# Kernel optimization log

Hardware: AMD Instinct MI355X
Metric: run time of the kernel (lower is better)

Reference implementation:

```python
import jax, jax.numpy as jnp
import numpy as np
import math

EPS = 1e-5  # torch LayerNorm default


def entmax15(z):
    # Peters & Martins exact sort-based alpha=1.5 entmax along last axis.
    z = z / 2.0
    z = z - jnp.max(z, axis=-1, keepdims=True)
    zs = -jnp.sort(-z, axis=-1)                      # descending
    K = z.shape[-1]
    rho = jnp.arange(1, K + 1, dtype=z.dtype)
    mean = jnp.cumsum(zs, axis=-1) / rho
    mean_sq = jnp.cumsum(zs * zs, axis=-1) / rho
    ss = rho * (mean_sq - mean * mean)
    delta = jnp.clip((1.0 - ss) / rho, 0.0)
    tau = mean - jnp.sqrt(delta)
    k = jnp.sum(tau <= zs, axis=-1, keepdims=True)   # support size
    tau_star = jnp.take_along_axis(tau, k - 1, axis=-1)
    p = jnp.square(jnp.clip(z - tau_star, 0.0))
    return p


def mish(x):
    return x * jnp.tanh(jax.nn.softplus(x))


def layer_norm(x, g, b):
    mu = jnp.mean(x, axis=-1, keepdims=True)
    var = jnp.var(x, axis=-1, keepdims=True)
    return (x - mu) / jnp.sqrt(var + EPS) * g + b


def setup_inputs() -> dict:
    key = jax.random.key(0)
    D, H, F = 512, 8, 2048
    B, S = 8, 1024
    ks = jax.random.split(key, 16)
    s = 1.0 / math.sqrt(D)
    inp = {
        "x": jax.random.normal(ks[0], (B, S, D), jnp.float32),
        # weights stored [in, out]; y = x @ W + b
        "Wq": jax.random.normal(ks[1], (D, D), jnp.float32) * s,
        "bq": jnp.zeros((D,), jnp.float32),
        "Wk": jax.random.normal(ks[2], (D, D), jnp.float32) * s,
        "bk": jnp.zeros((D,), jnp.float32),
        "Wv": jax.random.normal(ks[3], (D, D), jnp.float32) * s,
        "bv": jnp.zeros((D,), jnp.float32),
        "Wo": jax.random.normal(ks[4], (D, D), jnp.float32) * s,
        "bo": jnp.zeros((D,), jnp.float32),
        "g1": jnp.ones((D,), jnp.float32),
        "be1": jnp.zeros((D,), jnp.float32),
        "W1": jax.random.normal(ks[5], (D, F), jnp.float32) * s,
        "b1": jnp.zeros((F,), jnp.float32),
        "W2": jax.random.normal(ks[6], (F, D), jnp.float32) * (1.0 / math.sqrt(F)),
        "b2": jnp.zeros((D,), jnp.float32),
        "g2": jnp.ones((D,), jnp.float32),
        "be2": jnp.zeros((D,), jnp.float32),
    }
    return inp


def reference(x, Wq, bq, Wk, bk, Wv, bv, Wo, bo, g1, be1, W1, b1, W2, b2, g2, be2):
    B, S, D = x.shape
    H = 8
    hd = D // H
    # multi-head self-attention (z = x)
    q = (x @ Wq + bq).reshape(B, S, H, hd).transpose(0, 2, 1, 3)
    k = (x @ Wk + bk).reshape(B, S, H, hd).transpose(0, 2, 1, 3)
    v = (x @ Wv + bv).reshape(B, S, H, hd).transpose(0, 2, 1, 3)
    scores = jnp.einsum("bhqd,bhkd->bhqk", q, k) / math.sqrt(hd)
    attn = entmax15(scores)
    out = jnp.einsum("bhqk,bhkd->bhqd", attn, v)
    out = out.transpose(0, 2, 1, 3).reshape(B, S, D)
    y = out @ Wo + bo
    x = x + layer_norm(y, g1, be1)
    # feed-forward with Mish
    y = mish(x @ W1 + b1) @ W2 + b2
    x = x + layer_norm(y, g2, be2)
    return x
```

## Files before the change

### kernel.cpp

```cpp
#include <hip/hip_runtime.h>


typedef float f32x4 __attribute__((ext_vector_type(4)));
typedef float f32x2 __attribute__((ext_vector_type(2)));
typedef __bf16 b8 __attribute__((ext_vector_type(8)));

#define DEV static __device__ __forceinline__

DEV unsigned short f2bf(float f) {
  return __builtin_bit_cast(unsigned short, (__bf16)f);
}
DEV float bf2f(unsigned short b) { return __uint_as_float(((unsigned)b) << 16); }

DEV float mishf(float x) {
  if (x > 20.f) return x;
  float e = __expf(x);
  float u = 1.f + e;
  u *= u;
  return x * ((u - 1.f) / (u + 1.f));
}

DEV void async16(const void* g, void* l) {
  __builtin_amdgcn_global_load_lds(
      (const __attribute__((address_space(1))) unsigned int*)g,
      (__attribute__((address_space(3))) unsigned int*)l, 16, 0, 0);
}

DEV int mbcnt64(unsigned long long m) {
  return __builtin_amdgcn_mbcnt_hi((unsigned)(m >> 32),
                                   __builtin_amdgcn_mbcnt_lo((unsigned)m, 0));
}

template <int CTRL>
DEV float dppmov(float x) {
  return __builtin_bit_cast(
      float, __builtin_amdgcn_update_dpp(0, __builtin_bit_cast(int, x), CTRL,
                                         0xF, 0xF, true));
}
DEV float swz16(float x) {
  return __builtin_bit_cast(
      float, __builtin_amdgcn_ds_swizzle(__builtin_bit_cast(int, x), 0x401F));
}
DEV float wave_sum(float x) {
  x += dppmov<0xB1>(x);
  x += dppmov<0x4E>(x);
  x += dppmov<0x141>(x);
  x += dppmov<0x140>(x);
  x += swz16(x);
  x += __shfl_xor(x, 32);
  return x;
}
DEV float wave_max(float x) {
  x = fmaxf(x, dppmov<0xB1>(x));
  x = fmaxf(x, dppmov<0x4E>(x));
  x = fmaxf(x, dppmov<0x141>(x));
  x = fmaxf(x, dppmov<0x140>(x));
  x = fmaxf(x, swz16(x));
  x = fmaxf(x, __shfl_xor(x, 32));
  return x;
}

template <int WM, int WN, int EPI, bool OUTBF, bool DB>
__global__ __launch_bounds__(256) void gemm_bt(
    const unsigned short* __restrict__ A, const unsigned short* __restrict__ Bt,
    const float* __restrict__ bias, void* __restrict__ Cp,
    int K, int lda, int ldb, int ldc,
    long sA1, long sA2, long sB1, long sB2, long sC1, long sC2,
    int hdiv, float alpha) {
  constexpr int BM = WM * 64, BN = WN * 64;
  constexpr int NA = WM * 2, NB = WN * 2;
  constexpr int NBUF = DB ? 2 : 1;
  __shared__ unsigned short smA[NBUF * BM * 64];
  __shared__ unsigned short smB[NBUF * BN * 64];

  const int tid = threadIdx.x;
  const int lane = tid & 63;
  const int z = blockIdx.z;
  const long zi = z / hdiv, zr = z % hdiv;
  const unsigned short* Ab = A + zi * sA1 + zr * sA2 + (long)blockIdx.x * BM * lda;
  const unsigned short* Bb = Bt + zi * sB1 + zr * sB2 + (long)blockIdx.y * BN * ldb;

  int siA[NA];
  const unsigned short* gA[NA];
#pragma unroll
  for (int q = 0; q < NA; ++q) {
    int si = q * 256 + tid;
    int m = si >> 3, s = si & 7, g = s ^ (m & 7);
    siA[q] = si;
    gA[q] = Ab + (long)m * lda + g * 8;
  }
  int siB[NB];
  const unsigned short* gB[NB];
#pragma unroll
  for (int q = 0; q < NB; ++q) {
    int si = q * 256 + tid;
    int m = si >> 3, s = si & 7, g = s ^ (m & 7);
    siB[q] = si;
    gB[q] = Bb + (long)m * ldb + g * 8;
  }

  const int w = tid >> 6;
  const int wr = w / WN, wc = w % WN;
  const int fm = lane & 15, fg = lane >> 4;

  int aOff[4][2], bOff[4][2];
#pragma unroll
  for (int i = 0; i < 4; ++i)
#pragma unroll
    for (int ks = 0; ks < 2; ++ks) {
      int m = wr * 64 + i * 16 + fm;
      aOff[i][ks] = (m * 8 + ((ks * 4 + fg) ^ (fm & 7))) * 8;
      int n = wc * 64 + i * 16 + fm;
      bOff[i][ks] = (n * 8 + ((ks * 4 + fg) ^ (fm & 7))) * 8;
    }

  f32x4 acc[4][4];
#pragma unroll
  for (int i = 0; i < 4; ++i)
#pragma unroll
    for (int j = 0; j < 4; ++j) acc[i][j] = (f32x4){0.f, 0.f, 0.f, 0.f};

  auto stage = [&](int buf, int k0) {
    unsigned short* dA = smA + buf * (BM * 64);
    unsigned short* dB = smB + buf * (BN * 64);
#pragma unroll
    for (int q = 0; q < NA; ++q) async16(gA[q] + k0, (void*)&dA[siA[q] * 8]);
#pragma unroll
    for (int q = 0; q < NB; ++q) async16(gB[q] + k0, (void*)&dB[siB[q] * 8]);
  };
  auto compute = [&](int buf) {
    const unsigned short* sA = smA + buf * (BM * 64);
    const unsigned short* sB = smB + buf * (BN * 64);
#pragma unroll
    for (int ks = 0; ks < 2; ++ks) {
      b8 aF[4], bF[4];
#pragma unroll
      for (int i = 0; i < 4; ++i) aF[i] = *(const b8*)&sA[aOff[i][ks]];
#pragma unroll
      for (int j = 0; j < 4; ++j) bF[j] = *(const b8*)&sB[bOff[j][ks]];
#pragma unroll
      for (int i = 0; i < 4; ++i)
#pragma unroll
        for (int j = 0; j < 4; ++j)
          acc[i][j] = __builtin_amdgcn_mfma_f32_16x16x32_bf16(aF[i], bF[j], acc[i][j], 0, 0, 0);
    }
  };

  if constexpr (DB) {
    stage(0, 0);
    __syncthreads();
    int cur = 0;
    for (int k0 = 64; k0 < K; k0 += 64) {
      stage(cur ^ 1, k0);
      compute(cur);
      __syncthreads();
      cur ^= 1;
    }
    compute(cur);
  } else {
    for (int k0 = 0; k0 < K; k0 += 64) {
      __syncthreads();
      stage(0, k0);
      __syncthreads();
      compute(0);
    }
  }

  const long cbase = zi * sC1 + zr * sC2;
  const int row0 = blockIdx.x * BM + wr * 64 + fg * 4;
  const int col0 = blockIdx.y * BN + wc * 64 + fm;
#pragma unroll
  for (int i = 0; i < 4; ++i) {
#pragma unroll
    for (int j = 0; j < 4; ++j) {
      const int col = col0 + j * 16;
      float bv = (EPI >= 1) ? bias[col] : 0.f;
#pragma unroll
      for (int r = 0; r < 4; ++r) {
        const int row = row0 + i * 16 + r;
        float v = acc[i][j][r] * alpha + bv;
        if (EPI == 2) v = mishf(v);
        const long idx = cbase + (long)row * ldc + col;
        if constexpr (OUTBF)
          ((unsigned short*)Cp)[idx] = f2bf(v);
        else
          ((float*)Cp)[idx] = v;
      }
    }
  }
}

template <int NC>
DEV float solve_tau(const f32x2* zc, float tau) {
  int kprev = -1;
  const f32x2 zero2 = (f32x2){0.f, 0.f};
  for (int it = 0; it < 12; ++it) {
    const f32x2 t2 = (f32x2){tau, tau};
    f32x2 s1v = zero2, s2v = zero2;
    int k = 0;
#pragma unroll
    for (int i = 0; i < NC; ++i) {
      f32x2 h = zc[i] - t2;
      k += __popcll(__ballot(h.x > 0.f));
      k += __popcll(__ballot(h.y > 0.f));
      f32x2 hp = __builtin_elementwise_max(h, zero2);
      s1v += hp;
      s2v += hp * hp;
    }
    float s1 = wave_sum(s1v.x + s1v.y);
    float s2 = wave_sum(s2v.x + s2v.y);
    if (k == kprev) break;
    kprev = k;
    float kf = (float)k;
    float disc = fmaxf(fmaf(s1, s1, -kf * (s2 - 1.f)), 0.f);
    tau += (s1 - __builtin_sqrtf(disc)) / kf;
  }
  return tau;
}

DEV float solve_tau_lds(const float* cw, int nch, int lane, float tau) {
  int kprev = -1;
  const f32x2 zero2 = (f32x2){0.f, 0.f};
  for (int it = 0; it < 12; ++it) {
    const f32x2 t2 = (f32x2){tau, tau};
    f32x2 s1v = zero2, s2v = zero2;
    int k = 0;
    for (int c = 0; c < nch; ++c) {
      f32x2 h = *(const f32x2*)&cw[c * 128 + lane * 2] - t2;
      k += __popcll(__ballot(h.x > 0.f));
      k += __popcll(__ballot(h.y > 0.f));
      f32x2 hp = __builtin_elementwise_max(h, zero2);
      s1v += hp;
      s2v += hp * hp;
    }
    float s1 = wave_sum(s1v.x + s1v.y);
    float s2 = wave_sum(s2v.x + s2v.y);
    if (k == kprev) break;
    kprev = k;
    float kf = (float)k;
    float disc = fmaxf(fmaf(s1, s1, -kf * (s2 - 1.f)), 0.f);
    tau += (s1 - __builtin_sqrtf(disc)) / kf;
  }
  return tau;
}

__global__ __launch_bounds__(256) void entmax_rows(unsigned short* __restrict__ P) {
  const int tid = threadIdx.x, lane = tid & 63, wv = tid >> 6;
  const long row = (long)blockIdx.x * 4 + wv;
  unsigned short* p = P + row * 1024;
  __shared__ float cand[4][1024];

  union { uint4 v; unsigned short u[8]; } a, b;
  a.v = *(const uint4*)(p + lane * 16);
  b.v = *(const uint4*)(p + lane * 16 + 8);
  f32x2 zp[8];
#pragma unroll
  for (int i = 0; i < 4; ++i) {
    zp[i] = (f32x2){bf2f(a.u[2 * i]), bf2f(a.u[2 * i + 1])};
    zp[4 + i] = (f32x2){bf2f(b.u[2 * i]), bf2f(b.u[2 * i + 1])};
  }

  f32x2 mv = zp[0];
#pragma unroll
  for (int i = 1; i < 8; ++i) mv = __builtin_elementwise_max(mv, zp[i]);
  float m = wave_max(fmaxf(mv.x, mv.y));

  const float thr = m - 1.f;
  float* cw = cand[wv];

  int base = 0;
#pragma unroll
  for (int i = 0; i < 8; ++i) {
    unsigned long long mx = __ballot(zp[i].x > thr);
    if (zp[i].x > thr) cw[base + mbcnt64(mx)] = zp[i].x;
    base += __popcll(mx);
    unsigned long long my = __ballot(zp[i].y > thr);
    if (zp[i].y > thr) cw[base + mbcnt64(my)] = zp[i].y;
    base += __popcll(my);
  }

  const int nch = (base + 127) >> 7;
  for (int i = base + lane; i < nch * 128; i += 64) cw[i] = -1e30f;

  float tau;
  if (nch == 1) {
    f32x2 zc[1];
    zc[0] = *(const f32x2*)&cw[lane * 2];
    tau = solve_tau<1>(zc, thr);
  } else if (nch == 2) {
    f32x2 zc[2];
    zc[0] = *(const f32x2*)&cw[lane * 2];
    zc[1] = *(const f32x2*)&cw[128 + lane * 2];
    tau = solve_tau<2>(zc, thr);
  } else {
    tau = solve_tau_lds(cw, nch, lane, thr);
  }

  const f32x2 t2 = (f32x2){tau, tau};
  const f32x2 zero2 = (f32x2){0.f, 0.f};
#pragma unroll
  for (int i = 0; i < 4; ++i) {
    f32x2 h0 = __builtin_elementwise_max(zp[i] - t2, zero2);
    f32x2 h1 = __builtin_elementwise_max(zp[4 + i] - t2, zero2);
    f32x2 p0 = h0 * h0, p1 = h1 * h1;
    a.u[2 * i] = f2bf(p0.x);
    a.u[2 * i + 1] = f2bf(p0.y);
    b.u[2 * i] = f2bf(p1.x);
    b.u[2 * i + 1] = f2bf(p1.y);
  }
  *(uint4*)(p + lane * 16) = a.v;
  *(uint4*)(p + lane * 16 + 8) = b.v;
}

__global__ __launch_bounds__(256) void prep_all(
    const float* __restrict__ x, unsigned short* __restrict__ xb,
    const float* __restrict__ Wq, const float* __restrict__ Wk,
    const float* __restrict__ Wv, const float* __restrict__ Wo,
    const float* __restrict__ W1, const float* __restrict__ W2,
    unsigned short* __restrict__ Wqkvt, unsigned short* __restrict__ Wot,
    unsigned short* __restrict__ W1t, unsigned short* __restrict__ W2t,
    const float* __restrict__ bq, const float* __restrict__ bk,
    const float* __restrict__ bv, float* __restrict__ bqkv) {
  __shared__ float t[32][33];
  const int bid = blockIdx.x, tid = threadIdx.x;

  if (bid < 4096) {
    long i = ((long)bid * 256 + tid) * 4;
    float4 v = *(const float4*)&x[i];
    uint2 pk;
    pk.x = (unsigned)f2bf(v.x) | ((unsigned)f2bf(v.y) << 16);
    pk.y = (unsigned)f2bf(v.z) | ((unsigned)f2bf(v.w) << 16);
    *(uint2*)&xb[i] = pk;
    return;
  }

  const float* in;
  unsigned short* out;
  int ldi, ldo, bx, by;
  if (bid < 5120) {
    int t4 = (bid - 4096) >> 8, local = (bid - 4096) & 255;
    const float* ins[4] = {Wq, Wk, Wv, Wo};
    unsigned short* outs[4] = {Wqkvt, Wqkvt + 512 * 512, Wqkvt + 2 * 512 * 512, Wot};
    in = ins[t4];
    out = outs[t4];
    ldi = 512;
    ldo = 512;
    bx = local & 15;
    by = local >> 4;
  } else if (bid < 6144) {
    int local = bid - 5120;
    in = W1;
    out = W1t;
    ldi = 2048;
    ldo = 512;
    bx = local & 63;
    by = local >> 6;
  } else if (bid < 7168) {
    int local = bid - 6144;
    in = W2;
    out = W2t;
    ldi = 512;
    ldo = 2048;
    bx = local & 15;
    by = local >> 4;
  } else {
    int i = (bid - 7168) * 256 + tid;
    if (i < 512) bqkv[i] = bq[i];
    else if (i < 1024) bqkv[i] = bk[i - 512];
    else if (i < 1536) bqkv[i] = bv[i - 1024];
    return;
  }

  const int tx = tid & 31, ty = tid >> 5;
  const int r0 = by * 32, c0 = bx * 32;
#pragma unroll
  for (int q = 0; q < 4; ++q) {
    int r = ty + q * 8;
    t[r][tx] = in[(long)(r0 + r) * ldi + c0 + tx];
  }
  __syncthreads();
#pragma unroll
  for (int q = 0; q < 4; ++q) {
    int r = ty + q * 8;
    out[(long)(c0 + r) * ldo + r0 + tx] = f2bf(t[tx][r]);
  }
}

__global__ __launch_bounds__(256) void transpose_b2b(const unsigned short* __restrict__ in,
                                                     unsigned short* __restrict__ out,
                                                     int ldi, int ldo, long i1, long i2,
                                                     long o1, long o2, int hdiv) {
  __shared__ unsigned short t[32][33];
  const int z = blockIdx.z;
  in += (long)(z / hdiv) * i1 + (long)(z % hdiv) * i2;
  out += (long)(z / hdiv) * o1 + (long)(z % hdiv) * o2;
  const int tx = threadIdx.x & 31, ty = threadIdx.x >> 5;
  const int r0 = blockIdx.y * 32, c0 = blockIdx.x * 32;
#pragma unroll
  for (int q = 0; q < 4; ++q) {
    int r = ty + q * 8;
    t[r][tx] = in[(long)(r0 + r) * ldi + c0 + tx];
  }
  __syncthreads();
#pragma unroll
  for (int q = 0; q < 4; ++q) {
    int r = ty + q * 8;
    out[(long)(c0 + r) * ldo + r0 + tx] = t[tx][r];
  }
}

template <bool WB, int NS>
__global__ __launch_bounds__(256) void ln_res(const float* __restrict__ xin,
                                              const float* __restrict__ y, long ystr,
                                              const float* __restrict__ ybias,
                                              const float* __restrict__ g,
                                              const float* __restrict__ be,
                                              float* __restrict__ xo,
                                              unsigned short* __restrict__ xob) {
  const int row = blockIdx.x, tid = threadIdx.x, lane = tid & 63, wv = tid >> 6;
  const long base = (long)row * 512 + tid * 2;
  const int c = tid * 2;
  float2 v = *(const float2*)&y[base];
#pragma unroll
  for (int j = 1; j < NS; ++j) {
    float2 u = *(const float2*)&y[base + j * ystr];
    v.x += u.x;
    v.y += u.y;
  }
  v.x += ybias[c];
  v.y += ybias[c + 1];
  float s1 = wave_sum(v.x + v.y);
  float s2 = wave_sum(v.x * v.x + v.y * v.y);
  __shared__ float red[4][2];
  if (lane == 0) {
    red[wv][0] = s1;
    red[wv][1] = s2;
  }
  __syncthreads();
  s1 = red[0][0] + red[1][0] + red[2][0] + red[3][0];
  s2 = red[0][1] + red[1][1] + red[2][1] + red[3][1];
  const float mu = s1 * (1.f / 512.f);
  const float rstd = rsqrtf(s2 * (1.f / 512.f) - mu * mu + 1e-5f);
  float2 xv = *(const float2*)&xin[base];
  float o0 = xv.x + (v.x - mu) * rstd * g[c] + be[c];
  float o1 = xv.y + (v.y - mu) * rstd * g[c + 1] + be[c + 1];
  float2 ov;
  ov.x = o0;
  ov.y = o1;
  *(float2*)&xo[base] = ov;
  if constexpr (WB) {
    unsigned pk = (unsigned)f2bf(o0) | ((unsigned)f2bf(o1) << 16);
    *(unsigned*)&xob[base] = pk;
  }
}

extern "C" void kernel_launch(void* const* d_in, const int* in_sizes, int n_in,
                              void* d_out, int out_size, void* d_ws, size_t ws_size,
                              hipStream_t stream) {
  const int B = 8, S = 1024, D = 512, H = 8, F = 2048;
  const int BS = B * S;
  const int N3 = 3 * D;

  const float* x = (const float*)d_in[0];
  const float* Wq = (const float*)d_in[1];
  const float* bq = (const float*)d_in[2];
  const float* Wk = (const float*)d_in[3];
  const float* bk = (const float*)d_in[4];
  const float* Wv = (const float*)d_in[5];
  const float* bv = (const float*)d_in[6];
  const float* Wo = (const float*)d_in[7];
  const float* bo = (const float*)d_in[8];
  const float* g1 = (const float*)d_in[9];
  const float* be1 = (const float*)d_in[10];
  const float* W1 = (const float*)d_in[11];
  const float* b1 = (const float*)d_in[12];
  const float* W2 = (const float*)d_in[13];
  const float* b2 = (const float*)d_in[14];
  const float* g2 = (const float*)d_in[15];
  const float* be2 = (const float*)d_in[16];
  float* out = (float*)d_out;

  char* w = (char*)d_ws;
  size_t off = 0;
  auto alloc = [&](size_t bytes) -> void* {
    void* p = w + off;
    off += bytes;
    off = (off + 255) & ~(size_t)255;
    return p;
  };

  unsigned short* xb = (unsigned short*)alloc((size_t)BS * D * 2);
  unsigned short* Wqkvt = (unsigned short*)alloc((size_t)N3 * D * 2);
  unsigned short* Wot = (unsigned short*)alloc((size_t)D * D * 2);
  unsigned short* W1t = (unsigned short*)alloc((size_t)F * D * 2);
  unsigned short* W2t = (unsigned short*)alloc((size_t)D * F * 2);
  float* bqkv = (float*)alloc((size_t)N3 * 4);
  unsigned short* QKVb = (unsigned short*)alloc((size_t)BS * N3 * 2);
  unsigned short* Vt = (unsigned short*)alloc((size_t)BS * D * 2);
  unsigned short* attn = (unsigned short*)alloc((size_t)BS * D * 2);
  unsigned short* P = (unsigned short*)alloc((size_t)B * H * S * S * 2);
  float* x1 = (float*)alloc((size_t)BS * D * 4);
  unsigned short* hb = (unsigned short*)alloc((size_t)BS * F * 2);
  unsigned short* x1b = xb;
  float* yp = (float*)P;
  const long PSTR = (long)BS * D;

  const long SS = (long)S * S;
  const long HSS = (long)H * SS;

  prep_all<<<7174, 256, 0, stream>>>(x, xb, Wq, Wk, Wv, Wo, W1, W2,
                                     Wqkvt, Wot, W1t, W2t, bq, bk, bv, bqkv);

  gemm_bt<2, 2, 1, true, true><<<dim3(BS / 128, N3 / 128, 1), 256, 0, stream>>>(
      xb, Wqkvt, bqkv, QKVb, D, D, D, N3, 0, 0, 0, 0, 0, 0, 1, 1.f);

  transpose_b2b<<<dim3(2, 32, 64), 256, 0, stream>>>(
      QKVb + 1024, Vt, N3, S, (long)S * N3, 64, (long)8 * 64 * S, (long)64 * S, 8);

  gemm_bt<2, 2, 0, true, false><<<dim3(S / 128, S / 128, B * H), 256, 0, stream>>>(
      QKVb, QKVb + 512, nullptr, P, 64, N3, N3, S,
      (long)S * N3, 64, (long)S * N3, 64, HSS, SS, H, 1.f / 16.f);

  entmax_rows<<<(B * H * S) / 4, 256, 0, stream>>>(P);

  gemm_bt<4, 1, 0, true, true><<<dim3(S / 256, 1, B * H), 256, 0, stream>>>(
      P, Vt, nullptr, attn, S, S, S, D,
      HSS, SS, (long)8 * 64 * S, (long)64 * S, (long)S * D, 64, H, 1.f);

  gemm_bt<2, 2, 0, false, true><<<dim3(BS / 128, D / 128, 2), 256, 0, stream>>>(
      attn, Wot, nullptr, yp, D / 2, D, D, D, 0, D / 2, 0, D / 2, 0, PSTR, 2, 1.f);

  ln_res<true, 2><<<BS, 256, 0, stream>>>(x, yp, PSTR, bo, g1, be1, x1, x1b);

  gemm_bt<2, 2, 2, true, true><<<dim3(BS / 128, F / 128, 1), 256, 0, stream>>>(
      x1b, W1t, b1, hb, D, D, D, F, 0, 0, 0, 0, 0, 0, 1, 1.f);

  gemm_bt<2, 2, 0, false, true><<<dim3(BS / 128, D / 128, 2), 256, 0, stream>>>(
      hb, W2t, nullptr, yp, F / 2, F, F, D, 0, F / 2, 0, F / 2, 0, PSTR, 2, 1.f);

  ln_res<false, 2><<<BS, 256, 0, stream>>>(x1, yp, PSTR, b2, g2, be2, out, nullptr);
}
```

Baseline: 355.5 us.

## Fuse entmax probability transform into PV GEMM A-operand load

The entmax kernel now only solves for tau per row and writes it to a small buffer, instead of rewriting the full bf16 score matrix with the probabilities. A new PV GEMM reads the raw scores through registers, applies (z - tau)^2 clamped at zero while staging them into LDS, and multiplies with V. This removes one full write pass over the 128 MB score matrix. In exchange the A operand goes through registers rather than async LDS loads, which adds register pressure and ALU work inside the GEMM loop. The template flag on several other gemm_bt launches also changes, presumably a loading-mode choice.

```diff
diff --git a/kernel.cpp b/kernel.cpp
--- a/kernel.cpp
+++ b/kernel.cpp
@@ -185,6 +185,135 @@
           ((unsigned short*)Cp)[idx] = f2bf(v);
         else
           ((float*)Cp)[idx] = v;
+      }
+    }
+  }
+}
+
+__global__ __launch_bounds__(256) void gemm_pv(
+    const unsigned short* __restrict__ P, const unsigned short* __restrict__ Vt,
+    const float* __restrict__ Tau, unsigned short* __restrict__ attn) {
+  constexpr int BM = 256, BN = 64;
+  constexpr int NA = 8, NB = 2;
+  __shared__ unsigned short smA[2 * BM * 64];
+  __shared__ unsigned short smB[2 * BN * 64];
+
+  const int tid = threadIdx.x;
+  const int lane = tid & 63;
+  const int z = blockIdx.z;
+  const long SS = 1024L * 1024L;
+  const unsigned short* Ab = P + (long)z * SS + (long)blockIdx.x * BM * 1024;
+  const unsigned short* Bb = Vt + (long)z * 64 * 1024;
+  const float* Tb = Tau + (long)z * 1024 + blockIdx.x * BM;
+
+  int siA[NA];
+  const unsigned short* gA[NA];
+  float tq[NA];
+#pragma unroll
+  for (int q = 0; q < NA; ++q) {
+    int si = q * 256 + tid;
+    int m = si >> 3, s = si & 7, g = s ^ (m & 7);
+    siA[q] = si;
+    gA[q] = Ab + (long)m * 1024 + g * 8;
+    tq[q] = Tb[m];
+  }
+  int siB[NB];
+  const unsigned short* gB[NB];
+#pragma unroll
+  for (int q = 0; q < NB; ++q) {
+    int si = q * 256 + tid;
+    int m = si >> 3, s = si & 7, g = s ^ (m & 7);
+    siB[q] = si;
+    gB[q] = Bb + (long)m * 1024 + g * 8;
+  }
+
+  const int w = tid >> 6;
+  const int fm = lane & 15, fg = lane >> 4;
+  int aOff[4][2], bOff[4][2];
+#pragma unroll
+  for (int i = 0; i < 4; ++i)
+#pragma unroll
+    for (int ks = 0; ks < 2; ++ks) {
+      int m = w * 64 + i * 16 + fm;
+      aOff[i][ks] = (m * 8 + ((ks * 4 + fg) ^ (fm & 7))) * 8;
+      int n = i * 16 + fm;
+      bOff[i][ks] = (n * 8 + ((ks * 4 + fg) ^ (fm & 7))) * 8;
+    }
+
+  f32x4 acc[4][4];
+#pragma unroll
+  for (int i = 0; i < 4; ++i)
+#pragma unroll
+    for (int j = 0; j < 4; ++j) acc[i][j] = (f32x4){0.f, 0.f, 0.f, 0.f};
+
+  union AB { b8 v; unsigned short u[8]; };
+  AB areg[NA];
+  auto loadA = [&](int k0) {
+#pragma unroll
+    for (int q = 0; q < NA; ++q) areg[q].v = *(const b8*)(gA[q] + k0);
+  };
+  auto xformA = [&](int buf) {
+    unsigned short* dA = smA + buf * (BM * 64);
+#pragma unroll
+    for (int q = 0; q < NA; ++q) {
+      AB o;
+#pragma unroll
+      for (int e = 0; e < 8; ++e) {
+        float h = fmaxf(bf2f(areg[q].u[e]) - tq[q], 0.f);
+        o.u[e] = f2bf(h * h);
+      }
+      *(b8*)&dA[siA[q] * 8] = o.v;
+    }
+  };
+  auto stageB = [&](int buf, int k0) {
+    unsigned short* dB = smB + buf * (BN * 64);
+#pragma unroll
+    for (int q = 0; q < NB; ++q) async16(gB[q] + k0, (void*)&dB[siB[q] * 8]);
+  };
+  auto compute = [&](int buf) {
+    const unsigned short* sA = smA + buf * (BM * 64);
+    const unsigned short* sB = smB + buf * (BN * 64);
+#pragma unroll
+    for (int ks = 0; ks < 2; ++ks) {
+      b8 aF[4], bF[4];
+#pragma unroll
+      for (int i = 0; i < 4; ++i) aF[i] = *(const b8*)&sA[aOff[i][ks]];
+#pragma unroll
+      for (int j = 0; j < 4; ++j) bF[j] = *(const b8*)&sB[bOff[j][ks]];
+#pragma unroll
+      for (int i = 0; i < 4; ++i)
+#pragma unroll
+        for (int j = 0; j < 4; ++j)
+          acc[i][j] = __builtin_amdgcn_mfma_f32_16x16x32_bf16(aF[i], bF[j], acc[i][j], 0, 0, 0);
+    }
+  };
+
+  loadA(0);
+  stageB(0, 0);
+  xformA(0);
+  __syncthreads();
+  int cur = 0;
+  for (int k0 = 64; k0 < 1024; k0 += 64) {
+    loadA(k0);
+    stageB(cur ^ 1, k0);
+    compute(cur);
+    xformA(cur ^ 1);
+    __syncthreads();
+    cur ^= 1;
+  }
+  compute(cur);
+
+  const long cbase = (long)(z >> 3) * 1024 * 512 + (z & 7) * 64;
+  const int row0 = blockIdx.x * BM + w * 64 + fg * 4;
+#pragma unroll
+  for (int i = 0; i < 4; ++i) {
+#pragma unroll
+    for (int j = 0; j < 4; ++j) {
+      const int col = fm + j * 16;
+#pragma unroll
+      for (int r = 0; r < 4; ++r) {
+        const int row = row0 + i * 16 + r;
+        attn[cbase + (long)row * 512 + col] = f2bf(acc[i][j][r]);
       }
     }
   }
@@ -244,10 +373,11 @@
   return tau;
 }
 
-__global__ __launch_bounds__(256) void entmax_rows(unsigned short* __restrict__ P) {
+__global__ __launch_bounds__(256) void entmax_tau(const unsigned short* __restrict__ P,
+                                                  float* __restrict__ T) {
   const int tid = threadIdx.x, lane = tid & 63, wv = tid >> 6;
   const long row = (long)blockIdx.x * 4 + wv;
-  unsigned short* p = P + row * 1024;
+  const unsigned short* p = P + row * 1024;
   __shared__ float cand[4][1024];
 
   union { uint4 v; unsigned short u[8]; } a, b;
@@ -296,20 +426,7 @@
     tau = solve_tau_lds(cw, nch, lane, thr);
   }
 
-  const f32x2 t2 = (f32x2){tau, tau};
-  const f32x2 zero2 = (f32x2){0.f, 0.f};
-#pragma unroll
-  for (int i = 0; i < 4; ++i) {
-    f32x2 h0 = __builtin_elementwise_max(zp[i] - t2, zero2);
-    f32x2 h1 = __builtin_elementwise_max(zp[4 + i] - t2, zero2);
-    f32x2 p0 = h0 * h0, p1 = h1 * h1;
-    a.u[2 * i] = f2bf(p0.x);
-    a.u[2 * i + 1] = f2bf(p0.y);
-    b.u[2 * i] = f2bf(p1.x);
-    b.u[2 * i + 1] = f2bf(p1.y);
-  }
-  *(uint4*)(p + lane * 16) = a.v;
-  *(uint4*)(p + lane * 16 + 8) = b.v;
+  if (lane == 0) T[row] = tau;
 }
 
 __global__ __launch_bounds__(256) void prep_all(
@@ -499,6 +616,7 @@
   unsigned short* Vt = (unsigned short*)alloc((size_t)BS * D * 2);
   unsigned short* attn = (unsigned short*)alloc((size_t)BS * D * 2);
   unsigned short* P = (unsigned short*)alloc((size_t)B * H * S * S * 2);
+  float* Tau = (float*)alloc((size_t)B * H * S * 4);
   float* x1 = (float*)alloc((size_t)BS * D * 4);
   unsigned short* hb = (unsigned short*)alloc((size_t)BS * F * 2);
   unsigned short* x1b = xb;
@@ -511,7 +629,7 @@
   prep_all<<<7174, 256, 0, stream>>>(x, xb, Wq, Wk, Wv, Wo, W1, W2,
                                      Wqkvt, Wot, W1t, W2t, bq, bk, bv, bqkv);
 
-  gemm_bt<2, 2, 1, true, true><<<dim3(BS / 128, N3 / 128, 1), 256, 0, stream>>>(
+  gemm_bt<2, 2, 1, true, false><<<dim3(BS / 128, N3 / 128, 1), 256, 0, stream>>>(
       xb, Wqkvt, bqkv, QKVb, D, D, D, N3, 0, 0, 0, 0, 0, 0, 1, 1.f);
 
   transpose_b2b<<<dim3(2, 32, 64), 256, 0, stream>>>(
@@ -521,13 +639,11 @@
       QKVb, QKVb + 512, nullptr, P, 64, N3, N3, S,
       (long)S * N3, 64, (long)S * N3, 64, HSS, SS, H, 1.f / 16.f);
 
-  entmax_rows<<<(B * H * S) / 4, 256, 0, stream>>>(P);
-
-  gemm_bt<4, 1, 0, true, true><<<dim3(S / 256, 1, B * H), 256, 0, stream>>>(
-      P, Vt, nullptr, attn, S, S, S, D,
-      HSS, SS, (long)8 * 64 * S, (long)64 * S, (long)S * D, 64, H, 1.f);
-
-  gemm_bt<2, 2, 0, false, true><<<dim3(BS / 128, D / 128, 2), 256, 0, stream>>>(
+  entmax_tau<<<(B * H * S) / 4, 256, 0, stream>>>(P, Tau);
+
+  gemm_pv<<<dim3(S / 256, 1, B * H), 256, 0, stream>>>(P, Vt, Tau, attn);
+
+  gemm_bt<2, 2, 0, false, false><<<dim3(BS / 128, D / 128, 2), 256, 0, stream>>>(
       attn, Wot, nullptr, yp, D / 2, D, D, D, 0, D / 2, 0, D / 2, 0, PSTR, 2, 1.f);
 
   ln_res<true, 2><<<BS, 256, 0, stream>>>(x, yp, PSTR, bo, g1, be1, x1, x1b);
@@ -535,7 +651,7 @@
   gemm_bt<2, 2, 2, true, true><<<dim3(BS / 128, F / 128, 1), 256, 0, stream>>>(
       x1b, W1t, b1, hb, D, D, D, F, 0, 0, 0, 0, 0, 0, 1, 1.f);
 
-  gemm_bt<2, 2, 0, false, true><<<dim3(BS / 128, D / 128, 2), 256, 0, stream>>>(
+  gemm_bt<2, 2, 0, false, false><<<dim3(BS / 128, D / 128, 2), 256, 0, stream>>>(
       hb, W2t, nullptr, yp, F / 2, F, F, D, 0, F / 2, 0, F / 2, 0, PSTR, 2, 1.f);
 
   ln_res<false, 2><<<BS, 256, 0, stream>>>(x1, yp, PSTR, b2, g2, be2, out, nullptr);
```

Measured after the change: 339.1 us. -4.6%, faster.

## Fuse QK^T, entmax and PV into one attention kernel with LDS score tile

Applied to the files above, without the earlier changes.

Replaces the three-kernel attention path (score GEMM to a global bf16 P buffer, row-wise entmax, PV GEMM) with one kernel per 64-query tile. The kernel keeps the full 64x1024 score block in swizzled LDS, runs entmax in place, and then multiplies by double-buffered V tiles. This removes the large B*H*S*S global round trip of scores. It also switches the other GEMMs to single-buffered shared memory. The cost is 128KB+ of LDS per block, which allows very low occupancy, plus serialized phases within each block.

```diff
diff --git a/kernel.cpp b/kernel.cpp
--- a/kernel.cpp
+++ b/kernel.cpp
@@ -58,6 +58,34 @@
   x = fmaxf(x, swz16(x));
   x = fmaxf(x, __shfl_xor(x, 32));
   return x;
+}
+
+template <int NC>
+DEV float solve_tau(const f32x2* zc, float tau) {
+  int kprev = -1;
+  const f32x2 zero2 = (f32x2){0.f, 0.f};
+  for (int it = 0; it < 12; ++it) {
+    const f32x2 t2 = (f32x2){tau, tau};
+    f32x2 s1v = zero2, s2v = zero2;
+    int k = 0;
+#pragma unroll
+    for (int i = 0; i < NC; ++i) {
+      f32x2 h = zc[i] - t2;
+      k += __popcll(__ballot(h.x > 0.f));
+      k += __popcll(__ballot(h.y > 0.f));
+      f32x2 hp = __builtin_elementwise_max(h, zero2);
+      s1v += hp;
+      s2v += hp * hp;
+    }
+    float s1 = wave_sum(s1v.x + s1v.y);
+    float s2 = wave_sum(s2v.x + s2v.y);
+    if (k == kprev) break;
+    kprev = k;
+    float kf = (float)k;
+    float disc = fmaxf(fmaf(s1, s1, -kf * (s2 - 1.f)), 0.f);
+    tau += (s1 - __builtin_sqrtf(disc)) / kf;
+  }
+  return tau;
 }
 
 template <int WM, int WN, int EPI, bool OUTBF, bool DB>
@@ -190,126 +218,162 @@
   }
 }
 
-template <int NC>
-DEV float solve_tau(const f32x2* zc, float tau) {
-  int kprev = -1;
+__global__ __launch_bounds__(512) void attn_fused(
+    const unsigned short* __restrict__ QKV, const unsigned short* __restrict__ Vt,
+    unsigned short* __restrict__ attn) {
+  __shared__ unsigned short Sm[64 * 1024];
+  __shared__ unsigned short KV[2 * 64 * 64];
+
+  const int tid = threadIdx.x, lane = tid & 63, w = tid >> 6;
+  const int wr = w >> 1, wc = w & 1;
+  const int fm = lane & 15, fg = lane >> 4;
+  const int z = blockIdx.z, b = z >> 3, h = z & 7;
+  const int q0 = blockIdx.x * 64;
+  const long tokQ = (long)b * 1024 + q0;
+
+  b8 aQ[2];
+  {
+    const unsigned short* qp = QKV + (tokQ + wr * 16 + fm) * 1536 + h * 64 + fg * 8;
+    aQ[0] = *(const b8*)qp;
+    aQ[1] = *(const b8*)(qp + 32);
+  }
+
+  const int sm_ = tid >> 3, sg_ = (tid & 7) ^ (sm_ & 7);
+  const unsigned short* Ksrc =
+      QKV + ((long)b * 1024 + sm_) * 1536 + 512 + h * 64 + sg_ * 8;
+  const unsigned short* Vsrc = Vt + (long)z * 65536 + (long)sm_ * 1024 + sg_ * 8;
+  unsigned short* kvd[2] = {&KV[tid * 8], &KV[4096 + tid * 8]};
+
+  async16(Ksrc, kvd[0]);
+  __syncthreads();
+  for (int c = 0; c < 16; ++c) {
+    if (c + 1 < 16) async16(Ksrc + (long)(c + 1) * 64 * 1536, kvd[(c + 1) & 1]);
+    const unsigned short* kb = &KV[(c & 1) * 4096];
+#pragma unroll
+    for (int j = 0; j < 2; ++j) {
+      f32x4 acc = (f32x4){0.f, 0.f, 0.f, 0.f};
+#pragma unroll
+      for (int ks = 0; ks < 2; ++ks) {
+        const int n = wc * 32 + j * 16 + fm;
+        b8 bF = *(const b8*)&kb[(n * 8 + ((ks * 4 + fg) ^ (fm & 7))) * 8];
+        acc = __builtin_amdgcn_mfma_f32_16x16x32_bf16(aQ[ks], bF, acc, 0, 0, 0);
+      }
+#pragma unroll
+      for (int r = 0; r < 4; ++r) {
+        const int row = wr * 16 + fg * 4 + r;
+        const int col = c * 64 + wc * 32 + j * 16 + fm;
+        unsigned off = ((unsigned)(row * 1024 + col) * 2) ^ ((unsigned)(row & 7) << 4);
+        *(unsigned short*)((char*)Sm + off) = f2bf(acc[r] * 0.0625f);
+      }
+    }
+    __syncthreads();
+  }
+
+  float* scratch = (float*)KV + w * 512;
   const f32x2 zero2 = (f32x2){0.f, 0.f};
-  for (int it = 0; it < 12; ++it) {
+  for (int rr = 0; rr < 8; ++rr) {
+    const int row = w * 8 + rr;
+    const unsigned x = (unsigned)(row & 7) << 4;
+    const unsigned roff = (unsigned)(row * 1024 + lane * 16) * 2;
+    union { uint4 v; unsigned short u[8]; } a, bb;
+    a.v = *(const uint4*)((char*)Sm + (roff ^ x));
+    bb.v = *(const uint4*)((char*)Sm + ((roff + 16) ^ x));
+    f32x2 zp[8];
+#pragma unroll
+    for (int i = 0; i < 4; ++i) {
+      zp[i] = (f32x2){bf2f(a.u[2 * i]), bf2f(a.u[2 * i + 1])};
+      zp[4 + i] = (f32x2){bf2f(bb.u[2 * i]), bf2f(bb.u[2 * i + 1])};
+    }
+    f32x2 mv = zp[0];
+#pragma unroll
+    for (int i = 1; i < 8; ++i) mv = __builtin_elementwise_max(mv, zp[i]);
+    const float m = wave_max(fmaxf(mv.x, mv.y));
+    const float thr = m - 1.f;
+
+    int cnt = 0;
+#pragma unroll
+    for (int i = 0; i < 8; ++i) {
+      cnt += __popcll(__ballot(zp[i].x > thr));
+      cnt += __popcll(__ballot(zp[i].y > thr));
+    }
+    float tau;
+    if (cnt <= 256) {
+      int base = 0;
+#pragma unroll
+      for (int i = 0; i < 8; ++i) {
+        unsigned long long mx = __ballot(zp[i].x > thr);
+        if (zp[i].x > thr) scratch[base + mbcnt64(mx)] = zp[i].x;
+        base += __popcll(mx);
+        unsigned long long my = __ballot(zp[i].y > thr);
+        if (zp[i].y > thr) scratch[base + mbcnt64(my)] = zp[i].y;
+        base += __popcll(my);
+      }
+      const int nch = (base + 127) >> 7;
+      for (int i = base + lane; i < nch * 128; i += 64) scratch[i] = -1e30f;
+      if (nch == 1) {
+        f32x2 zc[1];
+        zc[0] = *(const f32x2*)&scratch[lane * 2];
+        tau = solve_tau<1>(zc, thr);
+      } else {
+        f32x2 zc[2];
+        zc[0] = *(const f32x2*)&scratch[lane * 2];
+        zc[1] = *(const f32x2*)&scratch[128 + lane * 2];
+        tau = solve_tau<2>(zc, thr);
+      }
+    } else {
+      tau = solve_tau<8>(zp, thr);
+    }
+
     const f32x2 t2 = (f32x2){tau, tau};
-    f32x2 s1v = zero2, s2v = zero2;
-    int k = 0;
-#pragma unroll
-    for (int i = 0; i < NC; ++i) {
-      f32x2 h = zc[i] - t2;
-      k += __popcll(__ballot(h.x > 0.f));
-      k += __popcll(__ballot(h.y > 0.f));
-      f32x2 hp = __builtin_elementwise_max(h, zero2);
-      s1v += hp;
-      s2v += hp * hp;
-    }
-    float s1 = wave_sum(s1v.x + s1v.y);
-    float s2 = wave_sum(s2v.x + s2v.y);
-    if (k == kprev) break;
-    kprev = k;
-    float kf = (float)k;
-    float disc = fmaxf(fmaf(s1, s1, -kf * (s2 - 1.f)), 0.f);
-    tau += (s1 - __builtin_sqrtf(disc)) / kf;
-  }
-  return tau;
-}
-
-DEV float solve_tau_lds(const float* cw, int nch, int lane, float tau) {
-  int kprev = -1;
-  const f32x2 zero2 = (f32x2){0.f, 0.f};
-  for (int it = 0; it < 12; ++it) {
-    const f32x2 t2 = (f32x2){tau, tau};
-    f32x2 s1v = zero2, s2v = zero2;
-    int k = 0;
-    for (int c = 0; c < nch; ++c) {
-      f32x2 h = *(const f32x2*)&cw[c * 128 + lane * 2] - t2;
-      k += __popcll(__ballot(h.x > 0.f));
-      k += __popcll(__ballot(h.y > 0.f));
-      f32x2 hp = __builtin_elementwise_max(h, zero2);
-      s1v += hp;
-      s2v += hp * hp;
-    }
-    float s1 = wave_sum(s1v.x + s1v.y);
-    float s2 = wave_sum(s2v.x + s2v.y);
-    if (k == kprev) break;
-    kprev = k;
-    float kf = (float)k;
-    float disc = fmaxf(fmaf(s1, s1, -kf * (s2 - 1.f)), 0.f);
-    tau += (s1 - __builtin_sqrtf(disc)) / kf;
-  }
-  return tau;
-}
-
-__global__ __launch_bounds__(256) void entmax_rows(unsigned short* __restrict__ P) {
-  const int tid = threadIdx.x, lane = tid & 63, wv = tid >> 6;
-  const long row = (long)blockIdx.x * 4 + wv;
-  unsigned short* p = P + row * 1024;
-  __shared__ float cand[4][1024];
-
-  union { uint4 v; unsigned short u[8]; } a, b;
-  a.v = *(const uint4*)(p + lane * 16);
-  b.v = *(const uint4*)(p + lane * 16 + 8);
-  f32x2 zp[8];
-#pragma unroll
-  for (int i = 0; i < 4; ++i) {
-    zp[i] = (f32x2){bf2f(a.u[2 * i]), bf2f(a.u[2 * i + 1])};
-    zp[4 + i] = (f32x2){bf2f(b.u[2 * i]), bf2f(b.u[2 * i + 1])};
-  }
-
-  f32x2 mv = zp[0];
-#pragma unroll
-  for (int i = 1; i < 8; ++i) mv = __builtin_elementwise_max(mv, zp[i]);
-  float m = wave_max(fmaxf(mv.x, mv.y));
-
-  const float thr = m - 1.f;
-  float* cw = cand[wv];
-
-  int base = 0;
-#pragma unroll
-  for (int i = 0; i < 8; ++i) {
-    unsigned long long mx = __ballot(zp[i].x > thr);
-    if (zp[i].x > thr) cw[base + mbcnt64(mx)] = zp[i].x;
-    base += __popcll(mx);
-    unsigned long long my = __ballot(zp[i].y > thr);
-    if (zp[i].y > thr) cw[base + mbcnt64(my)] = zp[i].y;
-    base += __popcll(my);
-  }
-
-  const int nch = (base + 127) >> 7;
-  for (int i = base + lane; i < nch * 128; i += 64) cw[i] = -1e30f;
-
-  float tau;
-  if (nch == 1) {
-    f32x2 zc[1];
-    zc[0] = *(const f32x2*)&cw[lane * 2];
-    tau = solve_tau<1>(zc, thr);
-  } else if (nch == 2) {
-    f32x2 zc[2];
-    zc[0] = *(const f32x2*)&cw[lane * 2];
-    zc[1] = *(const f32x2*)&cw[128 + lane * 2];
-    tau = solve_tau<2>(zc, thr);
-  } else {
-    tau = solve_tau_lds(cw, nch, lane, thr);
-  }
-
-  const f32x2 t2 = (f32x2){tau, tau};
-  const f32x2 zero2 = (f32x2){0.f, 0.f};
-#pragma unroll
-  for (int i = 0; i < 4; ++i) {
-    f32x2 h0 = __builtin_elementwise_max(zp[i] - t2, zero2);
-    f32x2 h1 = __builtin_elementwise_max(zp[4 + i] - t2, zero2);
-    f32x2 p0 = h0 * h0, p1 = h1 * h1;
-    a.u[2 * i] = f2bf(p0.x);
-    a.u[2 * i + 1] = f2bf(p0.y);
-    b.u[2 * i] = f2bf(p1.x);
-    b.u[2 * i + 1] = f2bf(p1.y);
-  }
-  *(uint4*)(p + lane * 16) = a.v;
-  *(uint4*)(p + lane * 16 + 8) = b.v;
+#pragma unroll
+    for (int i = 0; i < 4; ++i) {
+      f32x2 h0 = __builtin_elementwise_max(zp[i] - t2, zero2);
+      f32x2 h1 = __builtin_elementwise_max(zp[4 + i] - t2, zero2);
+      f32x2 p0 = h0 * h0, p1 = h1 * h1;
+      a.u[2 * i] = f2bf(p0.x);
+      a.u[2 * i + 1] = f2bf(p0.y);
+      bb.u[2 * i] = f2bf(p1.x);
+      bb.u[2 * i + 1] = f2bf(p1.y);
+    }
+    *(uint4*)((char*)Sm + (roff ^ x)) = a.v;
+    *(uint4*)((char*)Sm + ((roff + 16) ^ x)) = bb.v;
+  }
+  __syncthreads();
+
+  f32x4 accP[2];
+  accP[0] = (f32x4){0.f, 0.f, 0.f, 0.f};
+  accP[1] = (f32x4){0.f, 0.f, 0.f, 0.f};
+  async16(Vsrc, kvd[0]);
+  __syncthreads();
+  for (int c = 0; c < 16; ++c) {
+    if (c + 1 < 16) async16(Vsrc + (c + 1) * 64, kvd[(c + 1) & 1]);
+    const unsigned short* vb = &KV[(c & 1) * 4096];
+    b8 aP[2];
+#pragma unroll
+    for (int ks = 0; ks < 2; ++ks) {
+      const int row = wr * 16 + fm;
+      unsigned off = ((unsigned)(row * 1024 + c * 64 + (ks * 4 + fg) * 8) * 2) ^
+                     ((unsigned)(row & 7) << 4);
+      aP[ks] = *(const b8*)((char*)Sm + off);
+    }
+#pragma unroll
+    for (int j = 0; j < 2; ++j)
+#pragma unroll
+      for (int ks = 0; ks < 2; ++ks) {
+        const int n = wc * 32 + j * 16 + fm;
+        b8 bF = *(const b8*)&vb[(n * 8 + ((ks * 4 + fg) ^ (fm & 7))) * 8];
+        accP[j] = __builtin_amdgcn_mfma_f32_16x16x32_bf16(aP[ks], bF, accP[j], 0, 0, 0);
+      }
+    __syncthreads();
+  }
+
+  const long ob = tokQ * 512 + h * 64;
+#pragma unroll
+  for (int j = 0; j < 2; ++j)
+#pragma unroll
+    for (int r = 0; r < 4; ++r)
+      attn[ob + (long)(wr * 16 + fg * 4 + r) * 512 + wc * 32 + j * 16 + fm] =
+          f2bf(accP[j][r]);
 }
 
 __global__ __launch_bounds__(256) void prep_all(
@@ -498,44 +562,32 @@
   unsigned short* QKVb = (unsigned short*)alloc((size_t)BS * N3 * 2);
   unsigned short* Vt = (unsigned short*)alloc((size_t)BS * D * 2);
   unsigned short* attn = (unsigned short*)alloc((size_t)BS * D * 2);
-  unsigned short* P = (unsigned short*)alloc((size_t)B * H * S * S * 2);
+  float* yp = (float*)alloc((size_t)2 * BS * D * 4);
   float* x1 = (float*)alloc((size_t)BS * D * 4);
   unsigned short* hb = (unsigned short*)alloc((size_t)BS * F * 2);
   unsigned short* x1b = xb;
-  float* yp = (float*)P;
   const long PSTR = (long)BS * D;
-
-  const long SS = (long)S * S;
-  const long HSS = (long)H * SS;
 
   prep_all<<<7174, 256, 0, stream>>>(x, xb, Wq, Wk, Wv, Wo, W1, W2,
                                      Wqkvt, Wot, W1t, W2t, bq, bk, bv, bqkv);
 
-  gemm_bt<2, 2, 1, true, true><<<dim3(BS / 128, N3 / 128, 1), 256, 0, stream>>>(
+  gemm_bt<2, 2, 1, true, false><<<dim3(BS / 128, N3 / 128, 1), 256, 0, stream>>>(
       xb, Wqkvt, bqkv, QKVb, D, D, D, N3, 0, 0, 0, 0, 0, 0, 1, 1.f);
 
   transpose_b2b<<<dim3(2, 32, 64), 256, 0, stream>>>(
       QKVb + 1024, Vt, N3, S, (long)S * N3, 64, (long)8 * 64 * S, (long)64 * S, 8);
 
-  gemm_bt<2, 2, 0, true, false><<<dim3(S / 128, S / 128, B * H), 256, 0, stream>>>(
-      QKVb, QKVb + 512, nullptr, P, 64, N3, N3, S,
-      (long)S * N3, 64, (long)S * N3, 64, HSS, SS, H, 1.f / 16.f);
-
-  entmax_rows<<<(B * H * S) / 4, 256, 0, stream>>>(P);
-
-  gemm_bt<4, 1, 0, true, true><<<dim3(S / 256, 1, B * H), 256, 0, stream>>>(
-      P, Vt, nullptr, attn, S, S, S, D,
-      HSS, SS, (long)8 * 64 * S, (long)64 * S, (long)S * D, 64, H, 1.f);
-
-  gemm_bt<2, 2, 0, false, true><<<dim3(BS / 128, D / 128, 2), 256, 0, stream>>>(
+  attn_fused<<<dim3(S / 64, 1, B * H), 512, 0, stream>>>(QKVb, Vt, attn);
+
+  gemm_bt<2, 2, 0, false, false><<<dim3(BS / 128, D / 128, 2), 256, 0, stream>>>(
       attn, Wot, nullptr, yp, D / 2, D, D, D, 0, D / 2, 0, D / 2, 0, PSTR, 2, 1.f);
 
   ln_res<true, 2><<<BS, 256, 0, stream>>>(x, yp, PSTR, bo, g1, be1, x1, x1b);
 
-  gemm_bt<2, 2, 2, true, true><<<dim3(BS / 128, F / 128, 1), 256, 0, stream>>>(
+  gemm_bt<2, 2, 2, true, false><<<dim3(BS / 128, F / 128, 1), 256, 0, stream>>>(
       x1b, W1t, b1, hb, D, D, D, F, 0, 0, 0, 0, 0, 0, 1, 1.f);
 
-  gemm_bt<2, 2, 0, false, true><<<dim3(BS / 128, D / 128, 2), 256, 0, stream>>>(
+  gemm_bt<2, 2, 0, false, false><<<dim3(BS / 128, D / 128, 2), 256, 0, stream>>>(
       hb, W2t, nullptr, yp, F / 2, F, F, D, 0, F / 2, 0, F / 2, 0, PSTR, 2, 1.f);
 
   ln_res<false, 2><<<BS, 256, 0, stream>>>(x1, yp, PSTR, b2, g2, be2, out, nullptr);
```

After: 367.1 us. +3.2%, slower.
